# Kernel optimization log

Measured on AMD Instinct MI355X. Metric: run time of the kernel, lower is better.

Reference implementation:

```python
import jax, jax.numpy as jnp
import numpy as np

B, S, H = 2, 2048, 2048
NH = 16
Q_LORA = 1536
KV_LORA = 512
NOPE = 128
ROPE = 64
QHD = NOPE + ROPE  # 192
VHD = 128
FF = 8192
EPS = 1e-6
THETA = 10000.0


def rmsnorm(x, w, eps=EPS):
    var = jnp.mean(jnp.square(x), axis=-1, keepdims=True)
    return w * (x * jax.lax.rsqrt(var + eps))


def rotate_half(x):
    x1 = x[..., : x.shape[-1] // 2]
    x2 = x[..., x.shape[-1] // 2 :]
    return jnp.concatenate((-x2, x1), axis=-1)


def _deinterleave(x):
    # torch: x.view(b,h,s,d//2,2).transpose(0,1,2,4,3).reshape(b,h,s,d)
    b, h, s, d = x.shape
    return x.reshape(b, h, s, d // 2, 2).transpose(0, 1, 2, 4, 3).reshape(b, h, s, d)


def setup_inputs() -> dict:
    key = jax.random.key(0)
    ks = jax.random.split(key, 16)
    sc = 0.02
    # RoPE tables [S, ROPE]
    inv_freq = 1.0 / (THETA ** (np.arange(0, ROPE, 2, dtype=np.float64) / ROPE))
    freqs = np.outer(np.arange(S, dtype=np.float64), inv_freq)
    emb = np.concatenate([freqs, freqs], axis=-1)
    pos = jnp.sort(jax.random.randint(ks[15], (B, S), 0, S), axis=-1)
    return {
        "hidden_states": jax.random.normal(ks[0], (B, S, H), jnp.float32),
        "ln1_w": jnp.ones((H,), jnp.float32),
        "q_a_kernel": jax.random.normal(ks[1], (H, Q_LORA), jnp.float32) * sc,
        "q_a_ln_w": jnp.ones((Q_LORA,), jnp.float32),
        "q_b_kernel": jax.random.normal(ks[2], (Q_LORA, NH * QHD), jnp.float32) * sc,
        "kv_a_kernel": jax.random.normal(ks[3], (H, KV_LORA + ROPE), jnp.float32) * sc,
        "kv_a_ln_w": jnp.ones((KV_LORA,), jnp.float32),
        "kv_b_kernel": jax.random.normal(ks[4], (KV_LORA, NH * (NOPE + VHD)), jnp.float32) * sc,
        "o_kernel": jax.random.normal(ks[5], (NH * VHD, H), jnp.float32) * sc,
        "ln2_w": jnp.ones((H,), jnp.float32),
        "gate_kernel": jax.random.normal(ks[6], (H, FF), jnp.float32) * sc,
        "up_kernel": jax.random.normal(ks[7], (H, FF), jnp.float32) * sc,
        "down_kernel": jax.random.normal(ks[8], (FF, H), jnp.float32) * sc,
        "sin": jnp.asarray(np.sin(emb), jnp.float32),
        "cos": jnp.asarray(np.cos(emb), jnp.float32),
        "position_ids": pos,
    }


def reference(hidden_states, ln1_w, q_a_kernel, q_a_ln_w, q_b_kernel,
              kv_a_kernel, kv_a_ln_w, kv_b_kernel, o_kernel, ln2_w,
              gate_kernel, up_kernel, down_kernel, sin, cos, position_ids):
    b, s, h = hidden_states.shape
    x = rmsnorm(hidden_states, ln1_w)

    # --- MLA attention ---
    q = rmsnorm(x @ q_a_kernel, q_a_ln_w) @ q_b_kernel        # [b,s,NH*QHD]
    q = q.reshape(b, s, NH, QHD).transpose(0, 2, 1, 3)        # [b,NH,s,QHD]
    q_nope, q_pe = q[..., :NOPE], q[..., NOPE:]

    ckv = x @ kv_a_kernel                                     # [b,s,KV_LORA+ROPE]
    k_pe = ckv[..., KV_LORA:].reshape(b, s, 1, ROPE).transpose(0, 2, 1, 3)  # [b,1,s,ROPE]
    kv = rmsnorm(ckv[..., :KV_LORA], kv_a_ln_w) @ kv_b_kernel
    kv = kv.reshape(b, s, NH, NOPE + VHD).transpose(0, 2, 1, 3)
    k_nope = kv[..., :NOPE]
    v = kv[..., NOPE:]                                        # [b,NH,s,VHD]

    cos_e = cos[position_ids][:, None]                        # [b,1,s,ROPE]
    sin_e = sin[position_ids][:, None]
    q_pe = _deinterleave(q_pe)
    k_pe = _deinterleave(k_pe)
    q_pe = q_pe * cos_e + rotate_half(q_pe) * sin_e
    k_pe = k_pe * cos_e + rotate_half(k_pe) * sin_e

    qs = jnp.concatenate([q_nope, q_pe], axis=-1)             # [b,NH,s,QHD]
    ks = jnp.concatenate([k_nope, jnp.broadcast_to(k_pe, (b, NH, s, ROPE))], axis=-1)

    scale = QHD ** -0.5
    scores = jnp.einsum("bhqd,bhkd->bhqk", qs, ks) * scale
    causal = jnp.tril(jnp.ones((s, s), dtype=bool))
    scores = jnp.where(causal, scores, jnp.finfo(scores.dtype).min)
    probs = jax.nn.softmax(scores, axis=-1)
    attn = jnp.einsum("bhqk,bhkd->bhqd", probs, v)            # [b,NH,s,VHD]
    attn = attn.transpose(0, 2, 1, 3).reshape(b, s, NH * VHD)
    attn_out = attn @ o_kernel

    h1 = hidden_states + attn_out

    # --- dense MLP (SwiGLU) ---
    x2 = rmsnorm(h1, ln2_w)
    mlp = (jax.nn.silu(x2 @ gate_kernel) * (x2 @ up_kernel)) @ down_kernel
    return h1 + mlp
```

## Files before the change

kernel.cpp:

```cpp
#include <hip/hip_runtime.h>
#include <hip/hip_bf16.h>
#include <cstdint>

#define B_ 2
#define S_ 2048
#define H_ 2048
#define NH_ 16
#define QL_ 1536
#define KVL_ 512
#define NOPE_ 128
#define ROPE_ 64
#define QHD_ 192
#define VHD_ 128
#define FF_ 8192
#define BS_ (B_ * S_)
#define CKVP_ 640
#define KVW_ (NOPE_ + VHD_)

typedef __hip_bfloat16 bf16;
typedef __attribute__((ext_vector_type(8))) short short8_t;
typedef __attribute__((ext_vector_type(4))) float f32x4;

__device__ __forceinline__ float ldf(const float* p, size_t i) { return p[i]; }
__device__ __forceinline__ float ldf(const bf16* p, size_t i) { return __bfloat162float(p[i]); }
__device__ __forceinline__ void stf(float* p, size_t i, float v) { p[i] = v; }
__device__ __forceinline__ void stf(bf16* p, size_t i, float v) { p[i] = __float2bfloat16(v); }

__device__ __forceinline__ void gload16(const void* g, void* l)
{
    __builtin_amdgcn_global_load_lds((const unsigned int*)g, (unsigned int*)l, 16, 0, 0);
}

__global__ __launch_bounds__(256) void transp_bf16(
    const float* __restrict__ in, bf16* __restrict__ out, int K, int N, int Npad)
{
    __shared__ float t[32][33];
    const int n0 = blockIdx.x * 32, k0 = blockIdx.y * 32;
    for (int r = threadIdx.y; r < 32; r += 8) {
        const int n = n0 + threadIdx.x;
        t[r][threadIdx.x] = (n < N) ? in[(size_t)(k0 + r) * N + n] : 0.f;
    }
    __syncthreads();
    for (int r = threadIdx.y; r < 32; r += 8) {
        out[(size_t)(n0 + r) * K + k0 + threadIdx.x] = __float2bfloat16(t[threadIdx.x][r]);
    }
}

template<typename InT, typename OutT>
__global__ __launch_bounds__(256) void rmsnorm2(
    const InT* __restrict__ in, const float* __restrict__ w,
    OutT* __restrict__ out, int cols, int istride, int ostride)
{
    const int row = blockIdx.x;
    const InT* ip = in + (size_t)row * istride;
    OutT* op = out + (size_t)row * ostride;

    float ss = 0.f;
    for (int c = threadIdx.x; c < cols; c += 256) {
        float v = ldf(ip, c);
        ss = fmaf(v, v, ss);
    }
    #pragma unroll
    for (int off = 32; off; off >>= 1) ss += __shfl_xor(ss, off);
    __shared__ float red[4];
    if ((threadIdx.x & 63) == 0) red[threadIdx.x >> 6] = ss;
    __syncthreads();
    const float total = red[0] + red[1] + red[2] + red[3];
    const float scale = rsqrtf(total / (float)cols + 1e-6f);
    for (int c = threadIdx.x; c < cols; c += 256) {
        stf(op, c, ldf(ip, c) * scale * w[c]);
    }
}

template<int MODE, typename OutT>
__global__ __launch_bounds__(256) void gemm_bf16(
    const bf16* __restrict__ A, const bf16* __restrict__ BT,
    const float* __restrict__ Df, const bf16* __restrict__ Db,
    OutT* __restrict__ C, int M, int N, int K)
{
    __shared__ short As[128 * 32];
    __shared__ short Bs[128 * 32];
    const int tid = threadIdx.x;
    const int wid = tid >> 6, lane = tid & 63;
    const int bm = blockIdx.y * 128, bn = blockIdx.x * 128;
    const int wr = (wid >> 1) * 64, wc = (wid & 1) * 64;
    const int l16 = lane & 15;
    const int lk = (lane >> 4) << 3;

    f32x4 acc[4][4] = {};

    for (int k0 = 0; k0 < K; k0 += 32) {
        #pragma unroll
        for (int is = 0; is < 2; ++is) {
            const int c = is * 256 + tid;
            const int row = c >> 2;
            const int cb = (c & 3) * 16;
            const char* srcA = (const char*)A + ((size_t)(bm + row) * K + k0) * 2 + cb;
            const char* srcB = (const char*)BT + ((size_t)(bn + row) * K + k0) * 2 + cb;
            char* dstA = (char*)As + (is * 256 + wid * 64) * 16;
            char* dstB = (char*)Bs + (is * 256 + wid * 64) * 16;
            gload16(srcA, dstA);
            gload16(srcB, dstB);
        }
        __syncthreads();

        short8_t a[4], b[4];
        const short* ApW = As + (wr + l16) * 32 + lk;
        const short* BpW = Bs + (wc + l16) * 32 + lk;
        #pragma unroll
        for (int m = 0; m < 4; ++m) a[m] = *(const short8_t*)(ApW + m * 16 * 32);
        #pragma unroll
        for (int n = 0; n < 4; ++n) b[n] = *(const short8_t*)(BpW + n * 16 * 32);
        #pragma unroll
        for (int m = 0; m < 4; ++m)
            #pragma unroll
            for (int n = 0; n < 4; ++n)
                acc[m][n] = __builtin_amdgcn_mfma_f32_16x16x32_bf16(a[m], b[n], acc[m][n], 0, 0, 0);
        __syncthreads();
    }

    const int r0 = bm + wr + ((lane >> 4) << 2);
    const int c0 = bn + wc + l16;
    #pragma unroll
    for (int m = 0; m < 4; ++m) {
        #pragma unroll
        for (int n = 0; n < 4; ++n) {
            const int row = r0 + m * 16;
            const int col = c0 + n * 16;
            #pragma unroll
            for (int r = 0; r < 4; ++r) {
                const size_t off = (size_t)(row + r) * N + col;
                float v = acc[m][n][r];
                if (MODE == 1) v += Df[off];
                if (MODE == 2) {
                    const float g = __bfloat162float(Db[off]);
                    v *= g / (1.f + __expf(-g));
                }
                stf(C, off, v);
            }
        }
    }
}

template<int MODE, typename OutT>
__device__ __forceinline__ void epi_store(
    OutT* __restrict__ C, const float* __restrict__ Df, const bf16* __restrict__ Db,
    int N, int row, int col, float v)
{
    const size_t off = (size_t)row * N + col;
    if (MODE == 1) v += Df[off];
    if (MODE == 2) {
        const float g = __bfloat162float(Db[off]);
        v *= g / (1.f + __expf(-g));
    }
    stf(C, off, v);
}

__device__ __forceinline__ short8_t ldsfrag(const short* half_base, int r, int c)
{
    return *(const short8_t*)(half_base + r * 64 + ((c ^ (r & 7)) << 3));
}

template<int MODE, typename OutT>
__global__ __launch_bounds__(512, 2) void gemm256(
    const bf16* __restrict__ A, const bf16* __restrict__ BT,
    const float* __restrict__ Df, const bf16* __restrict__ Db,
    OutT* __restrict__ C, int M, int N, int K)
{
    __shared__ short lds[2][2][2][128 * 64];

    const int tid = threadIdx.x;
    const int wid = tid >> 6, lane = tid & 63;
    const int wm = wid >> 2, wn = wid & 3;
    const int l16 = lane & 15, hk = lane >> 4;

    const int nwg = gridDim.x * gridDim.y;
    const int orig = blockIdx.y * gridDim.x + blockIdx.x;
    const int q = nwg >> 3, r8 = nwg & 7;
    const int xcd = orig & 7, lid = orig >> 3;
    const int wg = (xcd < r8 ? xcd * (q + 1) : r8 * (q + 1) + (xcd - r8) * q) + lid;
    const int bn = (wg % gridDim.x) * 256;
    const int bm = (wg / gridDim.x) * 256;

    f32x4 acc[8][4] = {};
    const int nt = K >> 6;

    auto stage_half = [&](const bf16* gbase, short* lbase) {
        #pragma unroll
        for (int i = 0; i < 2; ++i) {
            const int ch = i * 512 + tid;
            const int row = ch >> 3, pc = ch & 7;
            const int gc = pc ^ (row & 7);
            const char* src = (const char*)(gbase + (size_t)row * K + gc * 8);
            char* dst = (char*)lbase + (i * 512 + wid * 64) * 16;
            gload16(src, dst);
        }
    };
    auto stage_tile = [&](int t, int buf) {
        const int k0 = t << 6;
        stage_half(A + (size_t)bm * K + k0,          &lds[buf][0][0][0]);
        stage_half(A + (size_t)(bm + 128) * K + k0,  &lds[buf][0][1][0]);
        stage_half(BT + (size_t)bn * K + k0,         &lds[buf][1][0][0]);
        stage_half(BT + (size_t)(bn + 128) * K + k0, &lds[buf][1][1][0]);
    };

    stage_tile(0, 0);
    stage_tile(1, 1);
    asm volatile("s_waitcnt vmcnt(8)" ::: "memory");
    __builtin_amdgcn_s_barrier();

    int cur = 0;
    for (int t = 0; t < nt; ++t) {
        const short* Ah = &lds[cur][0][wm][0];
        const short* Bh = &lds[cur][1][wn >> 1][0];
        const int brr = (wn & 1) * 64;

        short8_t bfr[4][2], afr[2][2];

        #pragma unroll
        for (int ph = 0; ph < 4; ++ph) {
            if (ph == 0) {
                #pragma unroll
                for (int nf = 0; nf < 4; ++nf)
                    #pragma unroll
                    for (int ks = 0; ks < 2; ++ks)
                        bfr[nf][ks] = ldsfrag(Bh, brr + nf * 16 + l16, ks * 4 + hk);
            }
            #pragma unroll
            for (int mi = 0; mi < 2; ++mi)
                #pragma unroll
                for (int ks = 0; ks < 2; ++ks)
                    afr[mi][ks] = ldsfrag(Ah, ph * 32 + mi * 16 + l16, ks * 4 + hk);
            __builtin_amdgcn_s_barrier();
            __builtin_amdgcn_s_setprio(1);
            #pragma unroll
            for (int mi = 0; mi < 2; ++mi)
                #pragma unroll
                for (int nf = 0; nf < 4; ++nf)
                    #pragma unroll
                    for (int ks = 0; ks < 2; ++ks)
                        acc[ph * 2 + mi][nf] = __builtin_amdgcn_mfma_f32_16x16x32_bf16(
                            afr[mi][ks], bfr[nf][ks], acc[ph * 2 + mi][nf], 0, 0, 0);
            __builtin_amdgcn_s_setprio(0);
        }

        __builtin_amdgcn_s_barrier();
        if (t + 2 < nt) {
            stage_tile(t + 2, cur);
            asm volatile("s_waitcnt vmcnt(8)" ::: "memory");
        } else if (t + 1 < nt) {
            asm volatile("s_waitcnt vmcnt(0)" ::: "memory");
        }
        __builtin_amdgcn_s_barrier();
        cur ^= 1;
    }

    const int r0 = bm + wm * 128 + (lane >> 4) * 4;
    const int c0 = bn + wn * 64 + l16;
    #pragma unroll
    for (int mf = 0; mf < 8; ++mf)
        #pragma unroll
        for (int nf = 0; nf < 4; ++nf)
            #pragma unroll
            for (int r = 0; r < 4; ++r)
                epi_store<MODE>(C, Df, Db, N, r0 + mf * 16 + r, c0 + nf * 16, acc[mf][nf][r]);
}

template<int MODE, typename OutT>
__global__ __launch_bounds__(512, 2) void gemm256n128(
    const bf16* __restrict__ A, const bf16* __restrict__ BT,
    const float* __restrict__ Df, const bf16* __restrict__ Db,
    OutT* __restrict__ C, int M, int N, int K)
{
    __shared__ short lds[2][3][128 * 64];

    const int tid = threadIdx.x;
    const int wid = tid >> 6, lane = tid & 63;
    const int wm = wid >> 1, wn = wid & 1;
    const int l16 = lane & 15, hk = lane >> 4;

    const int nwg = gridDim.x * gridDim.y;
    const int orig = blockIdx.y * gridDim.x + blockIdx.x;
    const int q = nwg >> 3, r8 = nwg & 7;
    const int xcd = orig & 7, lid = orig >> 3;
    const int wg = (xcd < r8 ? xcd * (q + 1) : r8 * (q + 1) + (xcd - r8) * q) + lid;
    const int bn = (wg % gridDim.x) * 128;
    const int bm = (wg / gridDim.x) * 256;

    f32x4 acc[4][4] = {};
    const int nt = K >> 6;

    auto stage_half = [&](const bf16* gbase, short* lbase) {
        #pragma unroll
        for (int i = 0; i < 2; ++i) {
            const int ch = i * 512 + tid;
            const int row = ch >> 3, pc = ch & 7;
            const int gc = pc ^ (row & 7);
            const char* src = (const char*)(gbase + (size_t)row * K + gc * 8);
            char* dst = (char*)lbase + (i * 512 + wid * 64) * 16;
            gload16(src, dst);
        }
    };
    auto stage_tile = [&](int t, int buf) {
        const int k0 = t << 6;
        stage_half(A + (size_t)bm * K + k0,          &lds[buf][0][0]);
        stage_half(A + (size_t)(bm + 128) * K + k0,  &lds[buf][1][0]);
        stage_half(BT + (size_t)bn * K + k0,         &lds[buf][2][0]);
    };

    stage_tile(0, 0);
    stage_tile(1, 1);
    asm volatile("s_waitcnt vmcnt(6)" ::: "memory");
    __builtin_amdgcn_s_barrier();

    int cur = 0;
    for (int t = 0; t < nt; ++t) {
        const short* Ah = &lds[cur][wm >> 1][0];
        const short* Bh = &lds[cur][2][0];
        const int arr = (wm & 1) * 64;
        const int brr = wn * 64;

        short8_t bfr[4][2], afr[2][2];

        #pragma unroll
        for (int ph = 0; ph < 2; ++ph) {
            if (ph == 0) {
                #pragma unroll
                for (int nf = 0; nf < 4; ++nf)
                    #pragma unroll
                    for (int ks = 0; ks < 2; ++ks)
                        bfr[nf][ks] = ldsfrag(Bh, brr + nf * 16 + l16, ks * 4 + hk);
            }
            #pragma unroll
            for (int mi = 0; mi < 2; ++mi)
                #pragma unroll
                for (int ks = 0; ks < 2; ++ks)
                    afr[mi][ks] = ldsfrag(Ah, arr + ph * 32 + mi * 16 + l16, ks * 4 + hk);
            __builtin_amdgcn_s_barrier();
            __builtin_amdgcn_s_setprio(1);
            #pragma unroll
            for (int mi = 0; mi < 2; ++mi)
                #pragma unroll
                for (int nf = 0; nf < 4; ++nf)
                    #pragma unroll
                    for (int ks = 0; ks < 2; ++ks)
                        acc[ph * 2 + mi][nf] = __builtin_amdgcn_mfma_f32_16x16x32_bf16(
                            afr[mi][ks], bfr[nf][ks], acc[ph * 2 + mi][nf], 0, 0, 0);
            __builtin_amdgcn_s_setprio(0);
        }

        __builtin_amdgcn_s_barrier();
        if (t + 2 < nt) {
            stage_tile(t + 2, cur);
            asm volatile("s_waitcnt vmcnt(6)" ::: "memory");
        } else if (t + 1 < nt) {
            asm volatile("s_waitcnt vmcnt(0)" ::: "memory");
        }
        __builtin_amdgcn_s_barrier();
        cur ^= 1;
    }

    const int r0 = bm + wm * 64 + (lane >> 4) * 4;
    const int c0 = bn + wn * 64 + l16;
    #pragma unroll
    for (int mf = 0; mf < 4; ++mf)
        #pragma unroll
        for (int nf = 0; nf < 4; ++nf)
            #pragma unroll
            for (int r = 0; r < 4; ++r)
                epi_store<MODE>(C, Df, Db, N, r0 + mf * 16 + r, c0 + nf * 16, acc[mf][nf][r]);
}

__global__ __launch_bounds__(512, 2) void gemm256dual(
    const bf16* __restrict__ A, const bf16* __restrict__ BG,
    const bf16* __restrict__ BU, bf16* __restrict__ C, int M, int N, int K)
{
    __shared__ short lds[2][4][128 * 64];

    const int tid = threadIdx.x;
    const int wid = tid >> 6, lane = tid & 63;
    const int wm = wid >> 1, wn = wid & 1;
    const int l16 = lane & 15, hk = lane >> 4;

    const int nwg = gridDim.x * gridDim.y;
    const int orig = blockIdx.y * gridDim.x + blockIdx.x;
    const int q = nwg >> 3, r8 = nwg & 7;
    const int xcd = orig & 7, lid = orig >> 3;
    const int wg = (xcd < r8 ? xcd * (q + 1) : r8 * (q + 1) + (xcd - r8) * q) + lid;
    const int bm = (wg % gridDim.y) * 256;
    const int bn = (wg / gridDim.y) * 128;

    f32x4 ag[4][4] = {}, au[4][4] = {};
    const int nt = K >> 6;

    auto stage_half = [&](const bf16* gbase, short* lbase) {
        #pragma unroll
        for (int i = 0; i < 2; ++i) {
            const int ch = i * 512 + tid;
            const int row = ch >> 3, pc = ch & 7;
            const int gc = pc ^ (row & 7);
            const char* src = (const char*)(gbase + (size_t)row * K + gc * 8);
            char* dst = (char*)lbase + (i * 512 + wid * 64) * 16;
            gload16(src, dst);
        }
    };

    stage_half(A + (size_t)bm * K,          &lds[0][0][0]);
    stage_half(A + (size_t)(bm + 128) * K,  &lds[0][1][0]);
    stage_half(BG + (size_t)bn * K,         &lds[0][2][0]);
    stage_half(BU + (size_t)bn * K,         &lds[0][3][0]);
    asm volatile("s_waitcnt vmcnt(0)" ::: "memory");
    __builtin_amdgcn_s_barrier();

    for (int t = 0; t < nt; ++t) {
        const int c = t & 1;
        const short* Ah = &lds[c][wm >> 1][0];
        const short* Gs = &lds[c][2][0];
        const short* Us = &lds[c][3][0];
        const int arr = (wm & 1) * 64;
        const int brr = wn * 64;
        const int k1 = (t + 1) << 6;

        short8_t gfr[4][2], ufr[4][2], afr[2][2];

        #pragma unroll
        for (int nf = 0; nf < 4; ++nf)
            #pragma unroll
            for (int ks = 0; ks < 2; ++ks) {
                gfr[nf][ks] = ldsfrag(Gs, brr + nf * 16 + l16, ks * 4 + hk);
                ufr[nf][ks] = ldsfrag(Us, brr + nf * 16 + l16, ks * 4 + hk);
            }
        #pragma unroll
        for (int mi = 0; mi < 2; ++mi)
            #pragma unroll
            for (int ks = 0; ks < 2; ++ks)
                afr[mi][ks] = ldsfrag(Ah, arr + mi * 16 + l16, ks * 4 + hk);
        if (t + 1 < nt) {
            stage_half(A + (size_t)bm * K + k1,         &lds[c ^ 1][0][0]);
            stage_half(A + (size_t)(bm + 128) * K + k1, &lds[c ^ 1][1][0]);
        }
        __builtin_amdgcn_s_setprio(1);
        #pragma unroll
        for (int mi = 0; mi < 2; ++mi)
            #pragma unroll
            for (int nf = 0; nf < 4; ++nf)
                #pragma unroll
                for (int ks = 0; ks < 2; ++ks) {
                    ag[mi][nf] = __builtin_amdgcn_mfma_f32_16x16x32_bf16(
                        afr[mi][ks], gfr[nf][ks], ag[mi][nf], 0, 0, 0);
                    au[mi][nf] = __builtin_amdgcn_mfma_f32_16x16x32_bf16(
                        afr[mi][ks], ufr[nf][ks], au[mi][nf], 0, 0, 0);
                }
        __builtin_amdgcn_s_setprio(0);
        __builtin_amdgcn_s_barrier();

        #pragma unroll
        for (int mi = 0; mi < 2; ++mi)
            #pragma unroll
            for (int ks = 0; ks < 2; ++ks)
                afr[mi][ks] = ldsfrag(Ah, arr + 32 + mi * 16 + l16, ks * 4 + hk);
        if (t + 1 < nt) {
            stage_half(BG + (size_t)bn * K + k1, &lds[c ^ 1][2][0]);
            stage_half(BU + (size_t)bn * K + k1, &lds[c ^ 1][3][0]);
        }
        __builtin_amdgcn_s_setprio(1);
        #pragma unroll
        for (int mi = 0; mi < 2; ++mi)
            #pragma unroll
            for (int nf = 0; nf < 4; ++nf)
                #pragma unroll
                for (int ks = 0; ks < 2; ++ks) {
                    ag[2 + mi][nf] = __builtin_amdgcn_mfma_f32_16x16x32_bf16(
                        afr[mi][ks], gfr[nf][ks], ag[2 + mi][nf], 0, 0, 0);
                    au[2 + mi][nf] = __builtin_amdgcn_mfma_f32_16x16x32_bf16(
                        afr[mi][ks], ufr[nf][ks], au[2 + mi][nf], 0, 0, 0);
                }
        __builtin_amdgcn_s_setprio(0);

        asm volatile("s_waitcnt vmcnt(0)" ::: "memory");
        __builtin_amdgcn_s_barrier();
    }

    const int r0 = bm + wm * 64 + (lane >> 4) * 4;
    const int c0 = bn + wn * 64 + l16;
    #pragma unroll
    for (int mf = 0; mf < 4; ++mf)
        #pragma unroll
        for (int nf = 0; nf < 4; ++nf)
            #pragma unroll
            for (int r = 0; r < 4; ++r) {
                const float gg = ag[mf][nf][r];
                const float uu = au[mf][nf][r];
                const float v = gg / (1.f + __expf(-gg)) * uu;
                C[(size_t)(r0 + mf * 16 + r) * N + c0 + nf * 16] = __float2bfloat16(v);
            }
}

__global__ __launch_bounds__(256) void rope_kernel(
    bf16* __restrict__ q, float* __restrict__ ckv,
    const int* __restrict__ pos_ids,
    const float* __restrict__ sinT, const float* __restrict__ cosT)
{
    const int wid = blockIdx.x * 4 + (threadIdx.x >> 6);
    const int lane = threadIdx.x & 63;
    const int NQ = BS_ * NH_;

    int bs;
    bf16* bptr = nullptr;
    float* fptr = nullptr;
    if (wid < NQ) {
        bs = wid >> 4;
        bptr = q + (size_t)wid * QHD_ + NOPE_;
    } else {
        bs = wid - NQ;
        fptr = ckv + (size_t)bs * CKVP_ + KVL_;
    }
    const int pos = pos_ids[bs];
    const float c  = cosT[pos * ROPE_ + lane];
    const float sn = sinT[pos * ROPE_ + lane];
    const float x = bptr ? __bfloat162float(bptr[lane]) : fptr[lane];
    const int j = lane & 31;
    const float x0 = __shfl(x, 2 * j);
    const float x1 = __shfl(x, 2 * j + 1);
    const float res = (lane < 32) ? fmaf(x0, c, -x1 * sn) : fmaf(x1, c, x0 * sn);
    if (bptr) bptr[lane] = __float2bfloat16(res);
    else      fptr[lane] = res;
}

__global__ __launch_bounds__(256) void pack_k(
    const float* __restrict__ KV, const float* __restrict__ CKV,
    bf16* __restrict__ Kh)
{
    const int total = BS_ * NH_ * (QHD_ / 2);
    for (int i = blockIdx.x * 256 + threadIdx.x; i < total; i += gridDim.x * 256) {
        const int d2 = i % (QHD_ / 2);
        const int t  = i / (QHD_ / 2);
        const int s  = t % S_;
        const int hh = (t / S_) % NH_;
        const int bb = t / (S_ * NH_);
        const int d = d2 * 2;
        float2 v;
        if (d < NOPE_) v = *(const float2*)&KV[(((size_t)bb * S_ + s) * NH_ + hh) * KVW_ + d];
        else           v = *(const float2*)&CKV[((size_t)bb * S_ + s) * CKVP_ + KVL_ + (d - NOPE_)];
        union { bf16 h[2]; unsigned int u; } cv;
        cv.h[0] = __float2bfloat16(v.x);
        cv.h[1] = __float2bfloat16(v.y);
        *(unsigned int*)&Kh[((size_t)(bb * NH_ + hh) * S_ + s) * QHD_ + d] = cv.u;
    }
}

__global__ __launch_bounds__(256) void pack_vt(
    const float* __restrict__ KV, bf16* __restrict__ Vt)
{
    __shared__ float t[32][33];
    const int s0 = blockIdx.x * 32, d0 = blockIdx.y * 32;
    const int bh = blockIdx.z;
    const int tx = threadIdx.x & 31, ty = threadIdx.x >> 5;
    for (int r = ty; r < 32; r += 8)
        t[r][tx] = KV[(((size_t)(bh >> 4) * S_ + s0 + r) * NH_ + (bh & 15)) * KVW_ + NOPE_ + d0 + tx];
    __syncthreads();
    for (int r = ty; r < 32; r += 8)
        Vt[((size_t)bh * VHD_ + d0 + r) * S_ + s0 + tx] = __float2bfloat16(t[tx][r]);
}

__global__ __launch_bounds__(512, 2) void attn_mfma(
    const bf16* __restrict__ Qp, const bf16* __restrict__ Kh,
    const bf16* __restrict__ Vt, bf16* __restrict__ outp)
{
    __shared__ __align__(16) short Ks[64][192];
    __shared__ __align__(16) short Vs[128][64];
    __shared__ __align__(16) short Ps[8][16][64];

    const int tid = threadIdx.x;
    const int wid = tid >> 6, lane = tid & 63;
    const int l16 = lane & 15;
    const int hk  = lane >> 4;
    const int lk  = hk << 3;
    const int pr  = hk << 2;
    const int lx  = l16 & 7;

    const int bid = blockIdx.x;
    const int orig = (bid & 7) * 64 + (bid >> 3);
    const int j  = orig & 15;
    const int gh = orig >> 4;
    const int h = gh & 15, b = gh >> 4;

    const int setB = wid >> 2;
    const int qblk = setB ? (31 - j) : j;
    const int qw = qblk * 64 + (wid & 3) * 16;
    const int myNt = qblk + 1;
    const int ntStage = 32 - j;

    short8_t qf[6];
    const bf16* qbase = Qp + (((size_t)b * S_ + qw + l16) * NH_ + h) * QHD_;
    #pragma unroll
    for (int kk = 0; kk < 6; ++kk)
        qf[kk] = *(const short8_t*)(qbase + kk * 32 + lk);

    const bf16* Khb = Kh + (size_t)(b * NH_ + h) * S_ * QHD_;
    const bf16* Vtb = Vt + (size_t)(b * NH_ + h) * VHD_ * S_;

    f32x4 o[8] = {};
    float mr[4] = {-3.0e38f, -3.0e38f, -3.0e38f, -3.0e38f};
    float lr[4] = {0.f, 0.f, 0.f, 0.f};
    const float scale = 0.07216878364870323f;

    const int krow = tid >> 3, kc0 = (tid & 7) * 3;
    const int vrow = tid >> 2, vc0 = (tid & 3) * 2;

    short8_t kreg[3], vreg[2];
    auto load_tile = [&](int kt) {
        const short* ksrc = (const short*)(Khb + ((size_t)(kt * 64 + krow)) * QHD_);
        kreg[0] = *(const short8_t*)(ksrc + (kc0 + 0) * 8);
        kreg[1] = *(const short8_t*)(ksrc + (kc0 + 1) * 8);
        kreg[2] = *(const short8_t*)(ksrc + (kc0 + 2) * 8);
        const short* vsrc = (const short*)(Vtb + (size_t)vrow * S_ + kt * 64);
        vreg[0] = *(const short8_t*)(vsrc + (vc0 + 0) * 8);
        vreg[1] = *(const short8_t*)(vsrc + (vc0 + 1) * 8);
    };
    auto write_tile = [&]() {
        const int kx = krow & 7, vx = vrow & 7;
        *(short8_t*)&Ks[krow][((kc0 + 0) ^ kx) << 3] = kreg[0];
        *(short8_t*)&Ks[krow][((kc0 + 1) ^ kx) << 3] = kreg[1];
        *(short8_t*)&Ks[krow][((kc0 + 2) ^ kx) << 3] = kreg[2];
        *(short8_t*)&Vs[vrow][((vc0 + 0) ^ vx) << 3] = vreg[0];
        *(short8_t*)&Vs[vrow][((vc0 + 1) ^ vx) << 3] = vreg[1];
    };

    load_tile(0);

    for (int t = 0; t < ntStage; ++t) {
        write_tile();
        __syncthreads();
        if (t + 1 < ntStage) load_tile(t + 1);
        if (t < myNt) {
            const int k0 = t << 6;
            f32x4 s[4] = {};
            #pragma unroll
            for (int kk = 0; kk < 6; ++kk) {
                #pragma unroll
                for (int n = 0; n < 4; ++n) {
                    short8_t kf = *(const short8_t*)&Ks[n * 16 + l16][((kk * 4 + hk) ^ lx) << 3];
                    s[n] = __builtin_amdgcn_mfma_f32_16x16x32_bf16(qf[kk], kf, s[n], 0, 0, 0);
                }
            }
            if (t == myNt - 1) {
                #pragma unroll
                for (int n = 0; n < 4; ++n) {
                    const int kg = k0 + n * 16 + l16;
                    #pragma unroll
                    for (int r = 0; r < 4; ++r) {
                        if (kg > qw + pr + r) s[n][r] = -3.0e38f;
                    }
                }
            }
            #pragma unroll
            for (int r = 0; r < 4; ++r) {
                float rm = fmaxf(fmaxf(s[0][r], s[1][r]), fmaxf(s[2][r], s[3][r]));
                rm = fmaxf(rm, __shfl_xor(rm, 1));
                rm = fmaxf(rm, __shfl_xor(rm, 2));
                rm = fmaxf(rm, __shfl_xor(rm, 4));
                rm = fmaxf(rm, __shfl_xor(rm, 8));
                const float mnew = fmaxf(mr[r], rm);
                const float corr = __expf((mr[r] - mnew) * scale);
                mr[r] = mnew;
                float rs = 0.f;
                #pragma unroll
                for (int n = 0; n < 4; ++n) {
                    const float p = __expf((s[n][r] - mnew) * scale);
                    s[n][r] = p;
                    rs += p;
                }
                rs += __shfl_xor(rs, 1);
                rs += __shfl_xor(rs, 2);
                rs += __shfl_xor(rs, 4);
                rs += __shfl_xor(rs, 8);
                lr[r] = lr[r] * corr + rs;
                #pragma unroll
                for (int n = 0; n < 8; ++n) o[n][r] *= corr;
            }
            #pragma unroll
            for (int n = 0; n < 4; ++n) {
                #pragma unroll
                for (int r = 0; r < 4; ++r) {
                    union { bf16 hh; short u; } cv;
                    cv.hh = __float2bfloat16(s[n][r]);
                    const int row = pr + r;
                    const int col = (((n * 2 + (l16 >> 3)) ^ (row & 7)) << 3) + (l16 & 7);
                    Ps[wid][row][col] = cv.u;
                }
            }
            #pragma unroll
            for (int kk2 = 0; kk2 < 2; ++kk2) {
                short8_t pf = *(const short8_t*)&Ps[wid][l16][((kk2 * 4 + hk) ^ lx) << 3];
                #pragma unroll
                for (int n = 0; n < 8; ++n) {
                    short8_t vf = *(const short8_t*)&Vs[n * 16 + l16][((kk2 * 4 + hk) ^ lx) << 3];
                    o[n] = __builtin_amdgcn_mfma_f32_16x16x32_bf16(pf, vf, o[n], 0, 0, 0);
                }
            }
        }
        __syncthreads();
    }

    float inv[4];
    #pragma unroll
    for (int r = 0; r < 4; ++r) inv[r] = 1.f / lr[r];
    bf16* ob = outp + (((size_t)b * S_ + qw + pr) * NH_ + h) * VHD_;
    #pragma unroll
    for (int r = 0; r < 4; ++r)
        #pragma unroll
        for (int n = 0; n < 8; ++n)
            ob[(size_t)r * (NH_ * VHD_) + n * 16 + l16] = __float2bfloat16(o[n][r] * inv[r]);
}

extern "C" void kernel_launch(void* const* d_in, const int* in_sizes, int n_in,
                              void* d_out, int out_size, void* d_ws, size_t ws_size,
                              hipStream_t stream)
{
    const float* hidden  = (const float*)d_in[0];
    const float* ln1_w   = (const float*)d_in[1];
    const float* q_a_k   = (const float*)d_in[2];
    const float* q_a_ln  = (const float*)d_in[3];
    const float* q_b_k   = (const float*)d_in[4];
    const float* kv_a_k  = (const float*)d_in[5];
    const float* kv_a_ln = (const float*)d_in[6];
    const float* kv_b_k  = (const float*)d_in[7];
    const float* o_k     = (const float*)d_in[8];
    const float* ln2_w   = (const float*)d_in[9];
    const float* gate_k  = (const float*)d_in[10];
    const float* up_k    = (const float*)d_in[11];
    const float* down_k  = (const float*)d_in[12];
    const float* sinT    = (const float*)d_in[13];
    const float* cosT    = (const float*)d_in[14];
    const int*   pos     = (const int*)d_in[15];
    float* out = (float*)d_out;
    char* ws = (char*)d_ws;

    bf16* qaT   = (bf16*)(ws + 0);
    bf16* qbT   = (bf16*)(ws + 6291456);
    bf16* kvaT  = (bf16*)(ws + 15728640);
    bf16* kvbT  = (bf16*)(ws + 18350080);
    bf16* oT    = (bf16*)(ws + 22544384);
    bf16* Xb    = (bf16*)(ws + 30932992);
    bf16* QAb   = (bf16*)(ws + 47710208);
    bf16* CKVNb = (bf16*)(ws + 60293120);
    bf16* Qb    = (bf16*)(ws + 64487424);
    float* CKV  = (float*)(ws + 89653248);
    float* KV   = (float*)(ws + 100139008);
    bf16* ATTNb = (bf16*)(ws + 167247872);
    bf16* Vt    = (bf16*)(ws + 0);
    bf16* Kh    = (bf16*)(ws + 30932992);
    bf16* gateT = (bf16*)(ws + 0);
    bf16* upT   = (bf16*)(ws + 33554432);
    bf16* downT = (bf16*)(ws + 67108864);
    bf16* X2b   = (bf16*)(ws + 100663296);
    bf16* MLPb  = (bf16*)(ws + 117440512);

    const dim3 tb(32, 8);

    transp_bf16<<<dim3(1536 / 32, 2048 / 32), tb, 0, stream>>>(q_a_k, qaT, 2048, 1536, 1536);
    transp_bf16<<<dim3(3072 / 32, 1536 / 32), tb, 0, stream>>>(q_b_k, qbT, 1536, 3072, 3072);
    transp_bf16<<<dim3(640 / 32, 2048 / 32), tb, 0, stream>>>(kv_a_k, kvaT, 2048, 576, 640);
    transp_bf16<<<dim3(4096 / 32, 512 / 32), tb, 0, stream>>>(kv_b_k, kvbT, 512, 4096, 4096);
    transp_bf16<<<dim3(2048 / 32, 2048 / 32), tb, 0, stream>>>(o_k, oT, 2048, 2048, 2048);

    rmsnorm2<float, bf16><<<BS_, 256, 0, stream>>>(hidden, ln1_w, Xb, H_, H_, H_);
    gemm_bf16<0, bf16><<<dim3(QL_ / 128, BS_ / 128), 256, 0, stream>>>(
        Xb, qaT, nullptr, nullptr, QAb, BS_, QL_, H_);
    rmsnorm2<bf16, bf16><<<BS_, 256, 0, stream>>>(QAb, q_a_ln, QAb, QL_, QL_, QL_);
    gemm256n128<0, bf16><<<dim3((NH_ * QHD_) / 128, BS_ / 256), 512, 0, stream>>>(
        QAb, qbT, nullptr, nullptr, Qb, BS_, NH_ * QHD_, QL_);
    gemm_bf16<0, float><<<dim3(CKVP_ / 128, BS_ / 128), 256, 0, stream>>>(
        Xb, kvaT, nullptr, nullptr, CKV, BS_, CKVP_, H_);
    rmsnorm2<float, bf16><<<BS_, 256, 0, stream>>>(CKV, kv_a_ln, CKVNb, KVL_, CKVP_, KVL_);
    gemm256<0, float><<<dim3((NH_ * KVW_) / 256, BS_ / 256), 512, 0, stream>>>(
        CKVNb, kvbT, nullptr, nullptr, KV, BS_, NH_ * KVW_, KVL_);
    rope_kernel<<<(BS_ * NH_ + BS_) / 4, 256, 0, stream>>>(Qb, CKV, pos, sinT, cosT);
    pack_k<<<2048, 256, 0, stream>>>(KV, CKV, Kh);
    pack_vt<<<dim3(S_ / 32, VHD_ / 32, B_ * NH_), 256, 0, stream>>>(KV, Vt);
    attn_mfma<<<dim3(512), 512, 0, stream>>>(Qb, Kh, Vt, ATTNb);
    gemm256n128<1, float><<<dim3(H_ / 128, BS_ / 256), 512, 0, stream>>>(
        ATTNb, oT, hidden, nullptr, out, BS_, H_, NH_ * VHD_);

    transp_bf16<<<dim3(8192 / 32, 2048 / 32), tb, 0, stream>>>(gate_k, gateT, 2048, 8192, 8192);
    transp_bf16<<<dim3(8192 / 32, 2048 / 32), tb, 0, stream>>>(up_k, upT, 2048, 8192, 8192);
    transp_bf16<<<dim3(2048 / 32, 8192 / 32), tb, 0, stream>>>(down_k, downT, 8192, 2048, 2048);

    rmsnorm2<float, bf16><<<BS_, 256, 0, stream>>>(out, ln2_w, X2b, H_, H_, H_);
    gemm256dual<<<dim3(FF_ / 128, BS_ / 256), 512, 0, stream>>>(
        X2b, gateT, upT, MLPb, BS_, FF_, H_);
    gemm256n128<1, float><<<dim3(H_ / 128, BS_ / 256), 512, 0, stream>>>(
        MLPb, downT, out, nullptr, out, BS_, H_, FF_);
}
```

Baseline: 978.3 us.

## Interleave prefetch into GEMM phases, fuse K packing into kv_b GEMM and RoPE

The two 256-row GEMM kernels move from a two-tiles-ahead staging scheme to a one-tile-ahead double buffer. Global loads for the next K tile are issued inside the compute phases, with a single wait at the end of each tile. The kv_b GEMM gets a new epilogue mode that writes k_nope straight into the packed bf16 K layout, and RoPE writes k_pe into all heads of that buffer, so the pack_k kernel is removed. The q_a projection also switches to the larger 256x128 tile kernel. The intent is to cut sync overhead and an extra pass over memory. The shallower prefetch depth may expose more load latency.

```diff
diff --git a/kernel.cpp b/kernel.cpp
--- a/kernel.cpp
+++ b/kernel.cpp
@@ -132,10 +132,6 @@
                 const size_t off = (size_t)(row + r) * N + col;
                 float v = acc[m][n][r];
                 if (MODE == 1) v += Df[off];
-                if (MODE == 2) {
-                    const float g = __bfloat162float(Db[off]);
-                    v *= g / (1.f + __expf(-g));
-                }
                 stf(C, off, v);
             }
         }
@@ -165,7 +161,7 @@
 __global__ __launch_bounds__(512, 2) void gemm256(
     const bf16* __restrict__ A, const bf16* __restrict__ BT,
     const float* __restrict__ Df, const bf16* __restrict__ Db,
-    OutT* __restrict__ C, int M, int N, int K)
+    OutT* __restrict__ C, bf16* __restrict__ KhO, int M, int N, int K)
 {
     __shared__ short lds[2][2][2][128 * 64];
 
@@ -196,24 +192,21 @@
             gload16(src, dst);
         }
     };
-    auto stage_tile = [&](int t, int buf) {
-        const int k0 = t << 6;
-        stage_half(A + (size_t)bm * K + k0,          &lds[buf][0][0][0]);
-        stage_half(A + (size_t)(bm + 128) * K + k0,  &lds[buf][0][1][0]);
-        stage_half(BT + (size_t)bn * K + k0,         &lds[buf][1][0][0]);
-        stage_half(BT + (size_t)(bn + 128) * K + k0, &lds[buf][1][1][0]);
-    };
-
-    stage_tile(0, 0);
-    stage_tile(1, 1);
-    asm volatile("s_waitcnt vmcnt(8)" ::: "memory");
+
+    stage_half(A + (size_t)bm * K,          &lds[0][0][0][0]);
+    stage_half(A + (size_t)(bm + 128) * K,  &lds[0][0][1][0]);
+    stage_half(BT + (size_t)bn * K,         &lds[0][1][0][0]);
+    stage_half(BT + (size_t)(bn + 128) * K, &lds[0][1][1][0]);
+    asm volatile("s_waitcnt vmcnt(0)" ::: "memory");
     __builtin_amdgcn_s_barrier();
 
-    int cur = 0;
     for (int t = 0; t < nt; ++t) {
-        const short* Ah = &lds[cur][0][wm][0];
-        const short* Bh = &lds[cur][1][wn >> 1][0];
+        const int c = t & 1;
+        const short* Ah = &lds[c][0][wm][0];
+        const short* Bh = &lds[c][1][wn >> 1][0];
         const int brr = (wn & 1) * 64;
+        const int k1 = (t + 1) << 6;
+        const bool pf = (t + 1 < nt);
 
         short8_t bfr[4][2], afr[2][2];
 
@@ -231,7 +224,15 @@
                 #pragma unroll
                 for (int ks = 0; ks < 2; ++ks)
                     afr[mi][ks] = ldsfrag(Ah, ph * 32 + mi * 16 + l16, ks * 4 + hk);
-            __builtin_amdgcn_s_barrier();
+            if (pf) {
+                if (ph == 0) {
+                    stage_half(A + (size_t)bm * K + k1,          &lds[c ^ 1][0][0][0]);
+                    stage_half(A + (size_t)(bm + 128) * K + k1,  &lds[c ^ 1][0][1][0]);
+                } else if (ph == 1) {
+                    stage_half(BT + (size_t)bn * K + k1,         &lds[c ^ 1][1][0][0]);
+                    stage_half(BT + (size_t)(bn + 128) * K + k1, &lds[c ^ 1][1][1][0]);
+                }
+            }
             __builtin_amdgcn_s_setprio(1);
             #pragma unroll
             for (int mi = 0; mi < 2; ++mi)
@@ -242,17 +243,9 @@
                         acc[ph * 2 + mi][nf] = __builtin_amdgcn_mfma_f32_16x16x32_bf16(
                             afr[mi][ks], bfr[nf][ks], acc[ph * 2 + mi][nf], 0, 0, 0);
             __builtin_amdgcn_s_setprio(0);
-        }
-
-        __builtin_amdgcn_s_barrier();
-        if (t + 2 < nt) {
-            stage_tile(t + 2, cur);
-            asm volatile("s_waitcnt vmcnt(8)" ::: "memory");
-        } else if (t + 1 < nt) {
-            asm volatile("s_waitcnt vmcnt(0)" ::: "memory");
-        }
-        __builtin_amdgcn_s_barrier();
-        cur ^= 1;
+            if (ph == 3) asm volatile("s_waitcnt vmcnt(0)" ::: "memory");
+            __builtin_amdgcn_s_barrier();
+        }
     }
 
     const int r0 = bm + wm * 128 + (lane >> 4) * 4;
@@ -262,8 +255,23 @@
         #pragma unroll
         for (int nf = 0; nf < 4; ++nf)
             #pragma unroll
-            for (int r = 0; r < 4; ++r)
-                epi_store<MODE>(C, Df, Db, N, r0 + mf * 16 + r, c0 + nf * 16, acc[mf][nf][r]);
+            for (int r = 0; r < 4; ++r) {
+                const int row = r0 + mf * 16 + r;
+                const int col = c0 + nf * 16;
+                float v = acc[mf][nf][r];
+                if (MODE == 3) {
+                    const int d = col & 255;
+                    if (d < NOPE_) {
+                        const int hh = col >> 8;
+                        const int bb = row >> 11, s = row & 2047;
+                        KhO[((size_t)(bb * NH_ + hh) * S_ + s) * QHD_ + d] = __float2bfloat16(v);
+                    } else {
+                        C[(size_t)row * N + col] = v;
+                    }
+                } else {
+                    epi_store<MODE>(C, Df, Db, N, row, col, v);
+                }
+            }
 }
 
 template<int MODE, typename OutT>
@@ -301,63 +309,68 @@
             gload16(src, dst);
         }
     };
-    auto stage_tile = [&](int t, int buf) {
-        const int k0 = t << 6;
-        stage_half(A + (size_t)bm * K + k0,          &lds[buf][0][0]);
-        stage_half(A + (size_t)(bm + 128) * K + k0,  &lds[buf][1][0]);
-        stage_half(BT + (size_t)bn * K + k0,         &lds[buf][2][0]);
-    };
-
-    stage_tile(0, 0);
-    stage_tile(1, 1);
-    asm volatile("s_waitcnt vmcnt(6)" ::: "memory");
+
+    stage_half(A + (size_t)bm * K,          &lds[0][0][0]);
+    stage_half(A + (size_t)(bm + 128) * K,  &lds[0][1][0]);
+    stage_half(BT + (size_t)bn * K,         &lds[0][2][0]);
+    asm volatile("s_waitcnt vmcnt(0)" ::: "memory");
     __builtin_amdgcn_s_barrier();
 
-    int cur = 0;
     for (int t = 0; t < nt; ++t) {
-        const short* Ah = &lds[cur][wm >> 1][0];
-        const short* Bh = &lds[cur][2][0];
+        const int c = t & 1;
+        const short* Ah = &lds[c][wm >> 1][0];
+        const short* Bh = &lds[c][2][0];
         const int arr = (wm & 1) * 64;
         const int brr = wn * 64;
+        const int k1 = (t + 1) << 6;
+        const bool pf = (t + 1 < nt);
 
         short8_t bfr[4][2], afr[2][2];
 
         #pragma unroll
-        for (int ph = 0; ph < 2; ++ph) {
-            if (ph == 0) {
-                #pragma unroll
-                for (int nf = 0; nf < 4; ++nf)
-                    #pragma unroll
-                    for (int ks = 0; ks < 2; ++ks)
-                        bfr[nf][ks] = ldsfrag(Bh, brr + nf * 16 + l16, ks * 4 + hk);
-            }
-            #pragma unroll
-            for (int mi = 0; mi < 2; ++mi)
+        for (int nf = 0; nf < 4; ++nf)
+            #pragma unroll
+            for (int ks = 0; ks < 2; ++ks)
+                bfr[nf][ks] = ldsfrag(Bh, brr + nf * 16 + l16, ks * 4 + hk);
+        #pragma unroll
+        for (int mi = 0; mi < 2; ++mi)
+            #pragma unroll
+            for (int ks = 0; ks < 2; ++ks)
+                afr[mi][ks] = ldsfrag(Ah, arr + mi * 16 + l16, ks * 4 + hk);
+        if (pf) {
+            stage_half(A + (size_t)bm * K + k1,         &lds[c ^ 1][0][0]);
+            stage_half(A + (size_t)(bm + 128) * K + k1, &lds[c ^ 1][1][0]);
+        }
+        __builtin_amdgcn_s_setprio(1);
+        #pragma unroll
+        for (int mi = 0; mi < 2; ++mi)
+            #pragma unroll
+            for (int nf = 0; nf < 4; ++nf)
                 #pragma unroll
                 for (int ks = 0; ks < 2; ++ks)
-                    afr[mi][ks] = ldsfrag(Ah, arr + ph * 32 + mi * 16 + l16, ks * 4 + hk);
-            __builtin_amdgcn_s_barrier();
-            __builtin_amdgcn_s_setprio(1);
-            #pragma unroll
-            for (int mi = 0; mi < 2; ++mi)
-                #pragma unroll
-                for (int nf = 0; nf < 4; ++nf)
-                    #pragma unroll
-                    for (int ks = 0; ks < 2; ++ks)
-                        acc[ph * 2 + mi][nf] = __builtin_amdgcn_mfma_f32_16x16x32_bf16(
-                            afr[mi][ks], bfr[nf][ks], acc[ph * 2 + mi][nf], 0, 0, 0);
-            __builtin_amdgcn_s_setprio(0);
-        }
-
+                    acc[mi][nf] = __builtin_amdgcn_mfma_f32_16x16x32_bf16(
+                        afr[mi][ks], bfr[nf][ks], acc[mi][nf], 0, 0, 0);
+        __builtin_amdgcn_s_setprio(0);
         __builtin_amdgcn_s_barrier();
-        if (t + 2 < nt) {
-            stage_tile(t + 2, cur);
-            asm volatile("s_waitcnt vmcnt(6)" ::: "memory");
-        } else if (t + 1 < nt) {
-            asm volatile("s_waitcnt vmcnt(0)" ::: "memory");
-        }
+
+        #pragma unroll
+        for (int mi = 0; mi < 2; ++mi)
+            #pragma unroll
+            for (int ks = 0; ks < 2; ++ks)
+                afr[mi][ks] = ldsfrag(Ah, arr + 32 + mi * 16 + l16, ks * 4 + hk);
+        if (pf) stage_half(BT + (size_t)bn * K + k1, &lds[c ^ 1][2][0]);
+        __builtin_amdgcn_s_setprio(1);
+        #pragma unroll
+        for (int mi = 0; mi < 2; ++mi)
+            #pragma unroll
+            for (int nf = 0; nf < 4; ++nf)
+                #pragma unroll
+                for (int ks = 0; ks < 2; ++ks)
+                    acc[2 + mi][nf] = __builtin_amdgcn_mfma_f32_16x16x32_bf16(
+                        afr[mi][ks], bfr[nf][ks], acc[2 + mi][nf], 0, 0, 0);
+        __builtin_amdgcn_s_setprio(0);
+        asm volatile("s_waitcnt vmcnt(0)" ::: "memory");
         __builtin_amdgcn_s_barrier();
-        cur ^= 1;
     }
 
     const int r0 = bm + wm * 64 + (lane >> 4) * 4;
@@ -497,8 +510,8 @@
 }
 
 __global__ __launch_bounds__(256) void rope_kernel(
-    bf16* __restrict__ q, float* __restrict__ ckv,
-    const int* __restrict__ pos_ids,
+    bf16* __restrict__ q, const float* __restrict__ ckv,
+    bf16* __restrict__ Kh, const int* __restrict__ pos_ids,
     const float* __restrict__ sinT, const float* __restrict__ cosT)
 {
     const int wid = blockIdx.x * 4 + (threadIdx.x >> 6);
@@ -506,46 +519,31 @@
     const int NQ = BS_ * NH_;
 
     int bs;
+    float x;
     bf16* bptr = nullptr;
-    float* fptr = nullptr;
     if (wid < NQ) {
         bs = wid >> 4;
         bptr = q + (size_t)wid * QHD_ + NOPE_;
+        x = __bfloat162float(bptr[lane]);
     } else {
         bs = wid - NQ;
-        fptr = ckv + (size_t)bs * CKVP_ + KVL_;
+        x = ckv[(size_t)bs * CKVP_ + KVL_ + lane];
     }
     const int pos = pos_ids[bs];
     const float c  = cosT[pos * ROPE_ + lane];
     const float sn = sinT[pos * ROPE_ + lane];
-    const float x = bptr ? __bfloat162float(bptr[lane]) : fptr[lane];
     const int j = lane & 31;
     const float x0 = __shfl(x, 2 * j);
     const float x1 = __shfl(x, 2 * j + 1);
     const float res = (lane < 32) ? fmaf(x0, c, -x1 * sn) : fmaf(x1, c, x0 * sn);
-    if (bptr) bptr[lane] = __float2bfloat16(res);
-    else      fptr[lane] = res;
-}
-
-__global__ __launch_bounds__(256) void pack_k(
-    const float* __restrict__ KV, const float* __restrict__ CKV,
-    bf16* __restrict__ Kh)
-{
-    const int total = BS_ * NH_ * (QHD_ / 2);
-    for (int i = blockIdx.x * 256 + threadIdx.x; i < total; i += gridDim.x * 256) {
-        const int d2 = i % (QHD_ / 2);
-        const int t  = i / (QHD_ / 2);
-        const int s  = t % S_;
-        const int hh = (t / S_) % NH_;
-        const int bb = t / (S_ * NH_);
-        const int d = d2 * 2;
-        float2 v;
-        if (d < NOPE_) v = *(const float2*)&KV[(((size_t)bb * S_ + s) * NH_ + hh) * KVW_ + d];
-        else           v = *(const float2*)&CKV[((size_t)bb * S_ + s) * CKVP_ + KVL_ + (d - NOPE_)];
-        union { bf16 h[2]; unsigned int u; } cv;
-        cv.h[0] = __float2bfloat16(v.x);
-        cv.h[1] = __float2bfloat16(v.y);
-        *(unsigned int*)&Kh[((size_t)(bb * NH_ + hh) * S_ + s) * QHD_ + d] = cv.u;
+    if (bptr) {
+        bptr[lane] = __float2bfloat16(res);
+    } else {
+        const int bb = bs >> 11, s = bs & 2047;
+        const bf16 rv = __float2bfloat16(res);
+        #pragma unroll
+        for (int hh = 0; hh < NH_; ++hh)
+            Kh[((size_t)(bb * NH_ + hh) * S_ + s) * QHD_ + NOPE_ + lane] = rv;
     }
 }
 
@@ -766,7 +764,7 @@
     transp_bf16<<<dim3(2048 / 32, 2048 / 32), tb, 0, stream>>>(o_k, oT, 2048, 2048, 2048);
 
     rmsnorm2<float, bf16><<<BS_, 256, 0, stream>>>(hidden, ln1_w, Xb, H_, H_, H_);
-    gemm_bf16<0, bf16><<<dim3(QL_ / 128, BS_ / 128), 256, 0, stream>>>(
+    gemm256n128<0, bf16><<<dim3(QL_ / 128, BS_ / 256), 512, 0, stream>>>(
         Xb, qaT, nullptr, nullptr, QAb, BS_, QL_, H_);
     rmsnorm2<bf16, bf16><<<BS_, 256, 0, stream>>>(QAb, q_a_ln, QAb, QL_, QL_, QL_);
     gemm256n128<0, bf16><<<dim3((NH_ * QHD_) / 128, BS_ / 256), 512, 0, stream>>>(
@@ -774,10 +772,9 @@
     gemm_bf16<0, float><<<dim3(CKVP_ / 128, BS_ / 128), 256, 0, stream>>>(
         Xb, kvaT, nullptr, nullptr, CKV, BS_, CKVP_, H_);
     rmsnorm2<float, bf16><<<BS_, 256, 0, stream>>>(CKV, kv_a_ln, CKVNb, KVL_, CKVP_, KVL_);
-    gemm256<0, float><<<dim3((NH_ * KVW_) / 256, BS_ / 256), 512, 0, stream>>>(
-        CKVNb, kvbT, nullptr, nullptr, KV, BS_, NH_ * KVW_, KVL_);
-    rope_kernel<<<(BS_ * NH_ + BS_) / 4, 256, 0, stream>>>(Qb, CKV, pos, sinT, cosT);
-    pack_k<<<2048, 256, 0, stream>>>(KV, CKV, Kh);
+    gemm256<3, float><<<dim3((NH_ * KVW_) / 256, BS_ / 256), 512, 0, stream>>>(
+        CKVNb, kvbT, nullptr, nullptr, KV, Kh, BS_, NH_ * KVW_, KVL_);
+    rope_kernel<<<(BS_ * NH_ + BS_) / 4, 256, 0, stream>>>(Qb, CKV, Kh, pos, sinT, cosT);
     pack_vt<<<dim3(S_ / 32, VHD_ / 32, B_ * NH_), 256, 0, stream>>>(KV, Vt);
     attn_mfma<<<dim3(512), 512, 0, stream>>>(Qb, Kh, Vt, ATTNb);
     gemm256n128<1, float><<<dim3(H_ / 128, BS_ / 256), 512, 0, stream>>>(
```

New measurement: 928.6 us. 5.1% less time.
